# Optimization experiments

Hardware: AMD Instinct MI355X
Metric: run time of the kernel (lower is better)

Reference implementation:

```python
import jax, jax.numpy as jnp
import numpy as np

B, S, D, H = 8, 4096, 1024, 12
BASE_FREQ = 432.0

def setup_inputs() -> dict:
    key = jax.random.key(0)
    k1, = jax.random.split(key, 1)
    x = jax.random.normal(k1, (B, S, D), dtype=jnp.float32)
    frequencies = BASE_FREQ * (jnp.arange(H, dtype=jnp.float32) + 1.0)
    amplitudes = jnp.ones((H,), dtype=jnp.float32)
    time = jnp.float32(0.0)
    return {"x": x, "frequencies": frequencies, "amplitudes": amplitudes, "time": time}

def reference(x, frequencies, amplitudes, time):
    # x: (B, S, D). resonance[b,t,d] = x[b,t,d] * mean_i amp_i*sin(2*pi*f_i*(time + t/S))
    Bx, Sx, Dx = x.shape
    Hn = frequencies.shape[0]
    t_frac = jnp.arange(Sx, dtype=x.dtype) / Sx            # (S,)
    phase = (2.0 * jnp.pi) * frequencies[:, None] * (time + t_frac[None, :])  # (H, S)
    wave = jnp.sum(amplitudes[:, None] * jnp.sin(phase), axis=0) / Hn         # (S,)
    return x * wave[None, :, None]
```

## Files before the change

kernel.cpp:

```cpp
#include <hip/hip_runtime.h>
#include <math.h>

#define D_DIM 1024
#define S_DIM 4096
#define F4_PER_ROW (D_DIM / 4)
#define ROWS_PER_BLOCK 4

#define TWO_PI     6.283185307179586476925286766559
#define INV_TWO_PI 0.159154943091895335768883763373

typedef float vfloat4 __attribute__((ext_vector_type(4)));

__global__ void ResonanceField_wave_kernel(const float* __restrict__ freq,
                                           const float* __restrict__ amp,
                                           const float* __restrict__ time_p,
                                           float* __restrict__ wave,
                                           int H, int S) {
    int t = blockIdx.x * blockDim.x + threadIdx.x;
    if (t >= S) return;
    double tf = (double)time_p[0] + (double)t / (double)S;
    double acc = 0.0;
    for (int i = 0; i < H; ++i) {
        double ph = TWO_PI * (double)freq[i] * tf;
        double r  = ph - TWO_PI * rint(ph * INV_TWO_PI);
        acc += (double)amp[i] * (double)sinf((float)r);
    }
    wave[t] = (float)(acc / (double)H);
}

__global__ void __launch_bounds__(256)
ResonanceField_scale_kernel(const vfloat4* __restrict__ x,
                            const float* __restrict__ wave,
                            vfloat4* __restrict__ out) {
    const int row0 = blockIdx.x * ROWS_PER_BLOCK;
    const int tid  = threadIdx.x;

    float   w[ROWS_PER_BLOCK];
    size_t  idx[ROWS_PER_BLOCK];
    vfloat4 v[ROWS_PER_BLOCK];

#pragma unroll
    for (int r = 0; r < ROWS_PER_BLOCK; ++r) {
        const int row = row0 + r;
        w[r]   = wave[row & (S_DIM - 1)];
        idx[r] = (size_t)row * F4_PER_ROW + tid;
        v[r]   = __builtin_nontemporal_load(&x[idx[r]]);
    }
#pragma unroll
    for (int r = 0; r < ROWS_PER_BLOCK; ++r) {
        v[r] *= w[r];
        __builtin_nontemporal_store(v[r], &out[idx[r]]);
    }
}

__global__ void ResonanceField_fused_kernel(const vfloat4* __restrict__ x,
                                            const float* __restrict__ freq,
                                            const float* __restrict__ amp,
                                            const float* __restrict__ time_p,
                                            vfloat4* __restrict__ out,
                                            int H) {
    const int t = blockIdx.x & (S_DIM - 1);
    const double tf = (double)time_p[0] + (double)t * (1.0 / (double)S_DIM);
    double acc = 0.0;
    for (int i = 0; i < H; ++i) {
        double ph = TWO_PI * (double)freq[i] * tf;
        double r  = ph - TWO_PI * rint(ph * INV_TWO_PI);
        acc += (double)amp[i] * (double)sinf((float)r);
    }
    const float w = (float)(acc / (double)H);
    const size_t idx = (size_t)blockIdx.x * blockDim.x + threadIdx.x;
    vfloat4 v = x[idx];
    v *= w;
    out[idx] = v;
}

extern "C" void kernel_launch(void* const* d_in, const int* in_sizes, int n_in,
                              void* d_out, int out_size, void* d_ws, size_t ws_size,
                              hipStream_t stream) {
    const float* x      = (const float*)d_in[0];
    const float* freq   = (const float*)d_in[1];
    const float* amp    = (const float*)d_in[2];
    const float* time_p = (const float*)d_in[3];
    float* out = (float*)d_out;

    const int H = in_sizes[1];
    const long long total = (long long)in_sizes[0];
    const int rows = (int)(total / D_DIM);
    const int threads = 256;

    if (ws_size >= (size_t)S_DIM * sizeof(float)) {
        float* wave = (float*)d_ws;
        ResonanceField_wave_kernel<<<(S_DIM + threads - 1) / threads, threads, 0, stream>>>(
            freq, amp, time_p, wave, H, S_DIM);
        ResonanceField_scale_kernel<<<rows / ROWS_PER_BLOCK, threads, 0, stream>>>(
            (const vfloat4*)x, wave, (vfloat4*)out);
    } else {
        ResonanceField_fused_kernel<<<rows, threads, 0, stream>>>(
            (const vfloat4*)x, freq, amp, time_p, (vfloat4*)out, H);
    }
}
```

Before: 228.9 us.

## Fuse wave computation into scale kernel with 8 rows per block

Drops the separate wave kernel and workspace round-trip. Each block now loads 8 rows of x up front, and the first 8 lanes of each wavefront compute the wave values for those rows in double precision. The values are then broadcast with shuffles and applied before nontemporal stores. This removes a launch and a dependent kernel boundary, at the cost of redundant per-block sin computation and more registers per thread.

```diff
diff --git a/kernel.cpp b/kernel.cpp
--- a/kernel.cpp
+++ b/kernel.cpp
@@ -4,68 +4,69 @@
 #define D_DIM 1024
 #define S_DIM 4096
 #define F4_PER_ROW (D_DIM / 4)
-#define ROWS_PER_BLOCK 4
+#define RPB 8
 
 #define TWO_PI     6.283185307179586476925286766559
 #define INV_TWO_PI 0.159154943091895335768883763373
 
 typedef float vfloat4 __attribute__((ext_vector_type(4)));
 
-__global__ void ResonanceField_wave_kernel(const float* __restrict__ freq,
-                                           const float* __restrict__ amp,
-                                           const float* __restrict__ time_p,
-                                           float* __restrict__ wave,
-                                           int H, int S) {
-    int t = blockIdx.x * blockDim.x + threadIdx.x;
-    if (t >= S) return;
-    double tf = (double)time_p[0] + (double)t / (double)S;
-    double acc = 0.0;
-    for (int i = 0; i < H; ++i) {
-        double ph = TWO_PI * (double)freq[i] * tf;
-        double r  = ph - TWO_PI * rint(ph * INV_TWO_PI);
-        acc += (double)amp[i] * (double)sinf((float)r);
+__global__ void __launch_bounds__(256)
+ResonanceField_fused8_kernel(const vfloat4* __restrict__ x,
+                             const float* __restrict__ freq,
+                             const float* __restrict__ amp,
+                             const float* __restrict__ time_p,
+                             vfloat4* __restrict__ out,
+                             int H) {
+    const int row0 = blockIdx.x * RPB;
+    const int tid  = threadIdx.x;
+    const size_t base = (size_t)row0 * F4_PER_ROW + tid;
+
+    vfloat4 v[RPB];
+#pragma unroll
+    for (int r = 0; r < RPB; ++r)
+        v[r] = __builtin_nontemporal_load(&x[base + (size_t)r * F4_PER_ROW]);
+
+    const int lane = tid & 63;
+    float wf = 0.0f;
+    if (lane < RPB) {
+        const int t = (row0 + lane) & (S_DIM - 1);
+        const double tf = (double)time_p[0] + (double)t * (1.0 / (double)S_DIM);
+        double acc = 0.0;
+        for (int i = 0; i < H; ++i) {
+            double ph = TWO_PI * (double)freq[i] * tf;
+            double rr = ph - TWO_PI * rint(ph * INV_TWO_PI);
+            acc += (double)amp[i] * (double)sinf((float)rr);
+        }
+        wf = (float)(acc / (double)H);
     }
-    wave[t] = (float)(acc / (double)H);
-}
 
-__global__ void __launch_bounds__(256)
-ResonanceField_scale_kernel(const vfloat4* __restrict__ x,
-                            const float* __restrict__ wave,
-                            vfloat4* __restrict__ out) {
-    const int row0 = blockIdx.x * ROWS_PER_BLOCK;
-    const int tid  = threadIdx.x;
-
-    float   w[ROWS_PER_BLOCK];
-    size_t  idx[ROWS_PER_BLOCK];
-    vfloat4 v[ROWS_PER_BLOCK];
+    float w[RPB];
+#pragma unroll
+    for (int r = 0; r < RPB; ++r)
+        w[r] = __shfl(wf, r);
 
 #pragma unroll
-    for (int r = 0; r < ROWS_PER_BLOCK; ++r) {
-        const int row = row0 + r;
-        w[r]   = wave[row & (S_DIM - 1)];
-        idx[r] = (size_t)row * F4_PER_ROW + tid;
-        v[r]   = __builtin_nontemporal_load(&x[idx[r]]);
-    }
-#pragma unroll
-    for (int r = 0; r < ROWS_PER_BLOCK; ++r) {
-        v[r] *= w[r];
-        __builtin_nontemporal_store(v[r], &out[idx[r]]);
+    for (int r = 0; r < RPB; ++r) {
+        vfloat4 t = v[r];
+        t *= w[r];
+        __builtin_nontemporal_store(t, &out[base + (size_t)r * F4_PER_ROW]);
     }
 }
 
-__global__ void ResonanceField_fused_kernel(const vfloat4* __restrict__ x,
-                                            const float* __restrict__ freq,
-                                            const float* __restrict__ amp,
-                                            const float* __restrict__ time_p,
-                                            vfloat4* __restrict__ out,
-                                            int H) {
+__global__ void ResonanceField_fused1_kernel(const vfloat4* __restrict__ x,
+                                             const float* __restrict__ freq,
+                                             const float* __restrict__ amp,
+                                             const float* __restrict__ time_p,
+                                             vfloat4* __restrict__ out,
+                                             int H) {
     const int t = blockIdx.x & (S_DIM - 1);
     const double tf = (double)time_p[0] + (double)t * (1.0 / (double)S_DIM);
     double acc = 0.0;
     for (int i = 0; i < H; ++i) {
         double ph = TWO_PI * (double)freq[i] * tf;
-        double r  = ph - TWO_PI * rint(ph * INV_TWO_PI);
-        acc += (double)amp[i] * (double)sinf((float)r);
+        double rr = ph - TWO_PI * rint(ph * INV_TWO_PI);
+        acc += (double)amp[i] * (double)sinf((float)rr);
     }
     const float w = (float)(acc / (double)H);
     const size_t idx = (size_t)blockIdx.x * blockDim.x + threadIdx.x;
@@ -88,14 +89,11 @@
     const int rows = (int)(total / D_DIM);
     const int threads = 256;
 
-    if (ws_size >= (size_t)S_DIM * sizeof(float)) {
-        float* wave = (float*)d_ws;
-        ResonanceField_wave_kernel<<<(S_DIM + threads - 1) / threads, threads, 0, stream>>>(
-            freq, amp, time_p, wave, H, S_DIM);
-        ResonanceField_scale_kernel<<<rows / ROWS_PER_BLOCK, threads, 0, stream>>>(
-            (const vfloat4*)x, wave, (vfloat4*)out);
+    if ((rows % RPB) == 0) {
+        ResonanceField_fused8_kernel<<<rows / RPB, threads, 0, stream>>>(
+            (const vfloat4*)x, freq, amp, time_p, (vfloat4*)out, H);
     } else {
-        ResonanceField_fused_kernel<<<rows, threads, 0, stream>>>(
+        ResonanceField_fused1_kernel<<<rows, threads, 0, stream>>>(
             (const vfloat4*)x, freq, amp, time_p, (vfloat4*)out, H);
     }
 }
```

Result: no change. 225.5 us, median of 2 (-1.5%).
